# Kernel tuning notes

Hardware: AMD Instinct MI355X
Metric: run time of the kernel (lower is better)

The kernel has to match this reference:

```python
import jax, jax.numpy as jnp
import numpy as np

B, T, C, H, HD, START = 2, 2048, 2048, 16, 128, 1024


def setup_inputs() -> dict:
    key = jax.random.key(0)
    ks = jax.random.split(key, 8)
    x = jax.random.normal(ks[0], (B, T, C), dtype=jnp.float32)
    k_cache = jax.random.normal(ks[1], (B, H, START, HD), dtype=jnp.float32)
    v_cache = jax.random.normal(ks[2], (B, H, START, HD), dtype=jnp.float32)
    wq = jax.random.normal(ks[3], (C, C), dtype=jnp.float32) * 0.02
    wk = jax.random.normal(ks[4], (C, C), dtype=jnp.float32) * 0.02
    wv = jax.random.normal(ks[5], (C, C), dtype=jnp.float32) * 0.02
    wo = jax.random.normal(ks[6], (C, C), dtype=jnp.float32) * 0.02
    return {"x": x, "k_cache": k_cache, "v_cache": v_cache,
            "wq": wq, "wk": wk, "wv": wv, "wo": wo, "start_pos": START}


def reference(x, k_cache, v_cache, wq, wk, wv, wo, start_pos):
    b, t, c = x.shape
    h = k_cache.shape[1]
    hd = c // h
    scale = hd ** -0.5
    # projections (torch Linear: y = x @ W^T), split heads -> [B,H,T,hd]
    def proj(w):
        return jnp.einsum('btc,dc->btd', x, w).reshape(b, t, h, hd).transpose(0, 2, 1, 3)
    q = proj(wq)
    k_new = proj(wk)
    v_new = proj(wv)
    # cache update: full K,V over [0, start_pos+T)
    k = jnp.concatenate([k_cache, k_new], axis=2)  # [B,H,S,hd]
    v = jnp.concatenate([v_cache, v_new], axis=2)
    s = k.shape[2]
    attn = jnp.einsum('bhtd,bhsd->bhts', q, k) * scale  # [B,H,T,S]
    # causal mask: query i (absolute pos start_pos+i) may attend to j <= start_pos+i
    mask = jnp.arange(s)[None, :] > (jnp.arange(t)[:, None] + start_pos)
    attn = jnp.where(mask, -jnp.inf, attn)
    attn = jax.nn.softmax(attn, axis=-1)
    out = jnp.einsum('bhts,bhsd->bhtd', attn, v)
    out = out.transpose(0, 2, 1, 3).reshape(b, t, c)
    return jnp.einsum('btc,dc->btd', out, wo)
```

## Files before the change

### kernel.cpp

```cpp
#include <hip/hip_runtime.h>
#include <stdint.h>

typedef unsigned short u16;
typedef __attribute__((ext_vector_type(8))) short short8;
typedef __attribute__((ext_vector_type(4))) float f32x4;
typedef __attribute__((ext_vector_type(4))) u16 us4;
typedef __attribute__((ext_vector_type(8))) u16 us8;

#define DEVI static __device__ __forceinline__

constexpr int BB = 2, TQ = 2048, CD = 2048, NH = 16, HD = 128;
constexpr int STARTP = 1024, SK = 3072;
constexpr int MM = BB * TQ;
constexpr float SM_SCALE = 0.08838834764831845f;

DEVI u16 f2bf(float f) {
  union { float f; unsigned u; } v; v.f = f;
  return (u16)((v.u + 0x7fffu + ((v.u >> 16) & 1u)) >> 16);
}

typedef __attribute__((address_space(1))) const unsigned int gas_u32;
typedef __attribute__((address_space(3))) unsigned int las_u32;

DEVI void gload16(const void* g, void* l) {
  __builtin_amdgcn_global_load_lds((gas_u32*)(uintptr_t)g,
                                   (las_u32*)(unsigned)(uintptr_t)l, 16, 0, 0);
}


__global__ __launch_bounds__(256) void cvt_k(const float* __restrict__ in,
                                             u16* __restrict__ out, int n4) {
  int i = blockIdx.x * 256 + threadIdx.x, st = gridDim.x * 256;
  for (; i < n4; i += st) {
    float4 v = *(const float4*)(in + (size_t)i * 4);
    us4 o = { f2bf(v.x), f2bf(v.y), f2bf(v.z), f2bf(v.w) };
    *(us4*)(out + (size_t)i * 4) = o;
  }
}

__global__ __launch_bounds__(256) void kcache_k(const float* __restrict__ kc,
                                                u16* __restrict__ Kb) {
  constexpr int n4 = BB * NH * STARTP * HD / 4;
  int i = blockIdx.x * 256 + threadIdx.x, st = gridDim.x * 256;
  for (; i < n4; i += st) {
    int e = i * 4;
    int bh = e / (STARTP * HD);
    int rem = e - bh * (STARTP * HD);
    float4 v = *(const float4*)(kc + e);
    us4 o = { f2bf(v.x), f2bf(v.y), f2bf(v.z), f2bf(v.w) };
    *(us4*)(Kb + (size_t)bh * SK * HD + rem) = o;
  }
}

__global__ __launch_bounds__(256) void vcache_t_k(const float* __restrict__ vc,
                                                  u16* __restrict__ Vt) {
  __shared__ float tl[64][128];
  const int bh = blockIdx.y;
  const int s0 = blockIdx.x * 64;
  const int tid = threadIdx.x;
  const float* src = vc + ((size_t)bh * STARTP + s0) * HD;
  for (int it = 0; it < 32; ++it) {
    int flat = it * 256 + tid;
    tl[flat >> 7][flat & 127] = src[flat];
  }
  __syncthreads();
  int d = tid >> 1, half = tid & 1;
  u16* dst = Vt + ((size_t)bh * HD + d) * SK + s0 + half * 32;
#pragma unroll
  for (int c = 0; c < 4; ++c) {
    us8 v;
#pragma unroll
    for (int j = 0; j < 8; ++j) v[j] = f2bf(tl[half * 32 + c * 8 + j][d]);
    *(us8*)(dst + c * 8) = v;
  }
}

template <int MODE>
__global__ __launch_bounds__(256) void gemm_nt(
    const u16* __restrict__ A, const u16* __restrict__ W0,
    const u16* __restrict__ W1, const u16* __restrict__ W2,
    u16* __restrict__ Qb, u16* __restrict__ Kb, u16* __restrict__ Vtb,
    float* __restrict__ Co) {
  __shared__ __align__(16) u16 Alds[128 * 32];
  __shared__ __align__(16) u16 Blds[128 * 32];
  const int tid = threadIdx.x, lane = tid & 63, w = tid >> 6;
  const int wr = w >> 1, wc = w & 1;
  const int l15 = lane & 15, l4 = lane >> 4;
  const int m0 = blockIdx.x * 128;
  const int tn = blockIdx.y;
  const u16* Wp;
  int which = 0, nb;
  if (MODE == 0) {
    which = tn >> 4;
    nb = (tn & 15) * 128;
    Wp = which == 0 ? W0 : (which == 1 ? W1 : W2);
  } else {
    nb = tn * 128;
    Wp = W0;
  }

  const char* Ab = (const char*)(A + (size_t)m0 * CD);
  const char* Wb = (const char*)(Wp + (size_t)nb * CD);

  f32x4 acc[4][4] = {};

  for (int kt = 0; kt < CD * 2; kt += 64) {
    __syncthreads();
#pragma unroll
    for (int c = 0; c < 2; ++c) {
      int o = (w * 2 + c) * 1024 + lane * 16;
      int row = o >> 6, ib = o & 63;
      gload16(Ab + (size_t)row * 4096 + kt + ib, (char*)Alds + o);
      gload16(Wb + (size_t)row * 4096 + kt + ib, (char*)Blds + o);
    }
    asm volatile("s_waitcnt vmcnt(0)" ::: "memory");
    __syncthreads();
    short8 af[4], bfr[4];
#pragma unroll
    for (int i = 0; i < 4; ++i) {
      af[i]  = *(const short8*)((const char*)Alds + (wr * 64 + i * 16 + l15) * 64 + l4 * 16);
      bfr[i] = *(const short8*)((const char*)Blds + (wc * 64 + i * 16 + l15) * 64 + l4 * 16);
    }
#pragma unroll
    for (int i = 0; i < 4; ++i)
#pragma unroll
      for (int j = 0; j < 4; ++j)
        acc[i][j] = __builtin_amdgcn_mfma_f32_16x16x32_bf16(af[i], bfr[j], acc[i][j], 0, 0, 0);
  }

  const int r0 = m0 + wr * 64;
  const int c0 = nb + wc * 64;
#pragma unroll
  for (int i = 0; i < 4; ++i) {
#pragma unroll
    for (int j = 0; j < 4; ++j) {
      int mrow = r0 + i * 16 + l4 * 4;
      int ncol = c0 + j * 16 + l15;
      if (MODE == 1) {
#pragma unroll
        for (int r = 0; r < 4; ++r)
          Co[(size_t)(mrow + r) * 2048 + ncol] = acc[i][j][r];
      } else {
        int b = mrow >> 11;
        int t = mrow & 2047;
        int h = ncol >> 7, d = ncol & 127;
        int bh = b * NH + h;
        if (which == 0) {
          u16* p = Qb + ((size_t)bh * TQ + t) * HD + d;
#pragma unroll
          for (int r = 0; r < 4; ++r) p[r * HD] = f2bf(acc[i][j][r]);
        } else if (which == 1) {
          u16* p = Kb + ((size_t)bh * SK + STARTP + t) * HD + d;
#pragma unroll
          for (int r = 0; r < 4; ++r) p[r * HD] = f2bf(acc[i][j][r]);
        } else {
          us4 v = { f2bf(acc[i][j][0]), f2bf(acc[i][j][1]),
                    f2bf(acc[i][j][2]), f2bf(acc[i][j][3]) };
          *(us4*)(Vtb + ((size_t)bh * HD + d) * SK + STARTP + t) = v;
        }
      }
    }
  }
}

__global__ __launch_bounds__(256, 2) void attn_k(const u16* __restrict__ Qb,
                                                 const u16* __restrict__ Kb,
                                                 const u16* __restrict__ Vtb,
                                                 u16* __restrict__ AO) {
  __shared__ __align__(16) u16 Klds[64 * 128];
  __shared__ __align__(16) u16 Vlds[128 * 64];
  __shared__ __align__(16) u16 Plds[4][32 * 64];
  const int tid = threadIdx.x, lane = tid & 63, w = tid >> 6;
  const int l15 = lane & 15, l4 = lane >> 4;
  const int qt0 = blockIdx.x * 128;
  const int bh = blockIdx.y;

  short8 qf[2][4];
  const u16* Qbase = Qb + ((size_t)bh * TQ + qt0 + w * 32) * HD;
#pragma unroll
  for (int mi = 0; mi < 2; ++mi)
#pragma unroll
    for (int ks = 0; ks < 4; ++ks)
      qf[mi][ks] = *(const short8*)(Qbase + (mi * 16 + l15) * HD + ks * 32 + l4 * 8);

  f32x4 acc[2][8] = {};
  float mrun[2][4], lrun[2][4];
#pragma unroll
  for (int mi = 0; mi < 2; ++mi)
#pragma unroll
    for (int r = 0; r < 4; ++r) { mrun[mi][r] = -__builtin_inff(); lrun[mi][r] = 0.f; }

  const int nfull = (STARTP + qt0) >> 6;
  const int ntiles = nfull + 2;
  const char* Kg = (const char*)(Kb + (size_t)bh * SK * HD);
  const char* Vg = (const char*)(Vtb + (size_t)bh * HD * SK);
  char* Pl = (char*)Plds[w];

  for (int tt = 0; tt < ntiles; ++tt) {
    const int s0 = tt << 6;
    __syncthreads();
#pragma unroll
    for (int c = 0; c < 4; ++c) {
      int o = (w * 4 + c) * 1024 + lane * 16;
      int a = o ^ (((o >> 8) & 7) << 4);
      gload16(Kg + (size_t)s0 * 256 + a, (char*)Klds + o);
    }
#pragma unroll
    for (int c = 0; c < 4; ++c) {
      int o = (w * 4 + c) * 1024 + lane * 16;
      int a = o ^ (((o >> 7) & 7) << 4);
      int row = a >> 7, ib = a & 127;
      gload16(Vg + ((size_t)row * SK + s0) * 2 + ib, (char*)Vlds + o);
    }
    asm volatile("s_waitcnt vmcnt(0)" ::: "memory");
    __syncthreads();

    f32x4 sa[2][4] = {};
#pragma unroll
    for (int ks = 0; ks < 4; ++ks) {
      short8 kf[4];
#pragma unroll
      for (int ni = 0; ni < 4; ++ni) {
        int row = l15 + ni * 16;
        int a = row * 256 + ks * 64 + l4 * 16;
        kf[ni] = *(const short8*)((const char*)Klds + (a ^ ((row & 7) << 4)));
      }
#pragma unroll
      for (int mi = 0; mi < 2; ++mi)
#pragma unroll
        for (int ni = 0; ni < 4; ++ni)
          sa[mi][ni] = __builtin_amdgcn_mfma_f32_16x16x32_bf16(qf[mi][ks], kf[ni], sa[mi][ni], 0, 0, 0);
    }

    const bool need_mask = (tt >= nfull);
#pragma unroll
    for (int mi = 0; mi < 2; ++mi)
#pragma unroll
      for (int ni = 0; ni < 4; ++ni)
#pragma unroll
        for (int r = 0; r < 4; ++r) {
          float v = sa[mi][ni][r] * SM_SCALE;
          if (need_mask) {
            int col = s0 + ni * 16 + l15;
            int lim = STARTP + qt0 + w * 32 + mi * 16 + l4 * 4 + r;
            if (col > lim) v = -__builtin_inff();
          }
          sa[mi][ni][r] = v;
        }

#pragma unroll
    for (int mi = 0; mi < 2; ++mi) {
#pragma unroll
      for (int r = 0; r < 4; ++r) {
        float tmax = fmaxf(fmaxf(sa[mi][0][r], sa[mi][1][r]),
                           fmaxf(sa[mi][2][r], sa[mi][3][r]));
        tmax = fmaxf(tmax, __shfl_xor(tmax, 1));
        tmax = fmaxf(tmax, __shfl_xor(tmax, 2));
        tmax = fmaxf(tmax, __shfl_xor(tmax, 4));
        tmax = fmaxf(tmax, __shfl_xor(tmax, 8));
        float mnew = fmaxf(mrun[mi][r], tmax);
        float sf = __expf(mrun[mi][r] - mnew);
        mrun[mi][r] = mnew;
        float rs = 0.f;
#pragma unroll
        for (int ni = 0; ni < 4; ++ni) {
          float p = __expf(sa[mi][ni][r] - mnew);
          sa[mi][ni][r] = p;
          rs += p;
        }
        rs += __shfl_xor(rs, 1);
        rs += __shfl_xor(rs, 2);
        rs += __shfl_xor(rs, 4);
        rs += __shfl_xor(rs, 8);
        lrun[mi][r] = lrun[mi][r] * sf + rs;
#pragma unroll
        for (int ni = 0; ni < 8; ++ni) acc[mi][ni][r] *= sf;
      }
    }

#pragma unroll
    for (int mi = 0; mi < 2; ++mi)
#pragma unroll
      for (int ni = 0; ni < 4; ++ni)
#pragma unroll
        for (int r = 0; r < 4; ++r) {
          int row = mi * 16 + l4 * 4 + r;
          int col = ni * 16 + l15;
          int a = row * 128 + col * 2;
          *(u16*)(Pl + (a ^ ((row & 7) << 4))) = f2bf(sa[mi][ni][r]);
        }

#pragma unroll
    for (int ks = 0; ks < 2; ++ks) {
      short8 pf[2], vf[8];
#pragma unroll
      for (int mi = 0; mi < 2; ++mi) {
        int row = l15 + mi * 16;
        int a = row * 128 + ks * 64 + l4 * 16;
        pf[mi] = *(const short8*)(Pl + (a ^ ((row & 7) << 4)));
      }
#pragma unroll
      for (int ni = 0; ni < 8; ++ni) {
        int row = l15 + ni * 16;
        int a = row * 128 + ks * 64 + l4 * 16;
        vf[ni] = *(const short8*)((const char*)Vlds + (a ^ ((row & 7) << 4)));
      }
#pragma unroll
      for (int mi = 0; mi < 2; ++mi)
#pragma unroll
        for (int ni = 0; ni < 8; ++ni)
          acc[mi][ni] = __builtin_amdgcn_mfma_f32_16x16x32_bf16(pf[mi], vf[ni], acc[mi][ni], 0, 0, 0);
    }
  }

  const int b = bh >> 4, h = bh & 15;
#pragma unroll
  for (int mi = 0; mi < 2; ++mi) {
#pragma unroll
    for (int r = 0; r < 4; ++r) {
      float inv = 1.f / lrun[mi][r];
      int t = qt0 + w * 32 + mi * 16 + l4 * 4 + r;
      u16* dst = AO + ((size_t)(b * TQ + t)) * CD + h * HD + l15;
#pragma unroll
      for (int ni = 0; ni < 8; ++ni)
        dst[ni * 16] = f2bf(acc[mi][ni][r] * inv);
    }
  }
}


extern "C" void kernel_launch(void* const* d_in, const int* in_sizes, int n_in,
                              void* d_out, int out_size, void* d_ws, size_t ws_size,
                              hipStream_t stream) {
  const float* x  = (const float*)d_in[0];
  const float* kc = (const float*)d_in[1];
  const float* vc = (const float*)d_in[2];
  const float* wq = (const float*)d_in[3];
  const float* wk = (const float*)d_in[4];
  const float* wv = (const float*)d_in[5];
  const float* wo = (const float*)d_in[6];
  float* out = (float*)d_out;
  char* ws = (char*)d_ws;

  u16* xbf = (u16*)(ws);
  u16* AO  = (u16*)(ws);
  u16* wqb = (u16*)(ws + 16777216);
  u16* wkb = (u16*)(ws + 25165824);
  u16* wvb = (u16*)(ws + 33554432);
  u16* wob = (u16*)(ws + 41943040);
  u16* Qb  = (u16*)(ws + 50331648);
  u16* Kb  = (u16*)(ws + 67108864);
  u16* Vtb = (u16*)(ws + 92274688);

  cvt_k<<<2048, 256, 0, stream>>>(x, xbf, MM * CD / 4);
  cvt_k<<<1024, 256, 0, stream>>>(wq, wqb, CD * CD / 4);
  cvt_k<<<1024, 256, 0, stream>>>(wk, wkb, CD * CD / 4);
  cvt_k<<<1024, 256, 0, stream>>>(wv, wvb, CD * CD / 4);
  cvt_k<<<1024, 256, 0, stream>>>(wo, wob, CD * CD / 4);
  kcache_k<<<2048, 256, 0, stream>>>(kc, Kb);
  vcache_t_k<<<dim3(16, 32), 256, 0, stream>>>(vc, Vtb);

  gemm_nt<0><<<dim3(32, 48), 256, 0, stream>>>(xbf, wqb, wkb, wvb, Qb, Kb, Vtb, nullptr);
  attn_k<<<dim3(16, 32), 256, 0, stream>>>(Qb, Kb, Vtb, AO);
  gemm_nt<1><<<dim3(32, 16), 256, 0, stream>>>(AO, wob, nullptr, nullptr,
                                               nullptr, nullptr, nullptr, out);
}
```

Measured before the change: 602.0 us.

## Rework attention with paired causal tiles, double-buffered K/V, and lazy rescaling

The attention kernel now handles two 64-row query tiles per block, pairing tile qp with tile 31-qp so every block does the same amount of causal work. K/V tiles are double-buffered in LDS so the next tile's loads are issued while the current tile is computed. Softmax works in base 2 with exp2 and the scale folded in, and it only rescales the running max and accumulators when the new max exceeds the old by a threshold. The cost is smaller per-wave tiles (16 rows per wave), which lowers MFMA reuse of the loaded K/V, plus double the LDS and some extra control flow.

```diff
diff --git a/kernel.cpp b/kernel.cpp
--- a/kernel.cpp
+++ b/kernel.cpp
@@ -13,6 +13,7 @@
 constexpr int STARTP = 1024, SK = 3072;
 constexpr int MM = BB * TQ;
 constexpr float SM_SCALE = 0.08838834764831845f;
+constexpr float QSL2 = SM_SCALE * 1.4426950408889634f;
 
 DEVI u16 f2bf(float f) {
   union { float f; unsigned u; } v; v.f = f;
@@ -167,55 +168,90 @@
                                                  const u16* __restrict__ Kb,
                                                  const u16* __restrict__ Vtb,
                                                  u16* __restrict__ AO) {
-  __shared__ __align__(16) u16 Klds[64 * 128];
-  __shared__ __align__(16) u16 Vlds[128 * 64];
-  __shared__ __align__(16) u16 Plds[4][32 * 64];
+  __shared__ __align__(16) u16 Klds[2][64 * 128];
+  __shared__ __align__(16) u16 Vlds[2][128 * 64];
+  __shared__ __align__(16) u16 Plds[4][16 * 64];
   const int tid = threadIdx.x, lane = tid & 63, w = tid >> 6;
   const int l15 = lane & 15, l4 = lane >> 4;
-  const int qt0 = blockIdx.x * 128;
-  const int bh = blockIdx.y;
-
-  short8 qf[2][4];
-  const u16* Qbase = Qb + ((size_t)bh * TQ + qt0 + w * 32) * HD;
-#pragma unroll
-  for (int mi = 0; mi < 2; ++mi)
-#pragma unroll
-    for (int ks = 0; ks < 4; ++ks)
-      qf[mi][ks] = *(const short8*)(Qbase + (mi * 16 + l15) * HD + ks * 32 + l4 * 8);
-
-  f32x4 acc[2][8] = {};
-  float mrun[2][4], lrun[2][4];
-#pragma unroll
-  for (int mi = 0; mi < 2; ++mi)
-#pragma unroll
-    for (int r = 0; r < 4; ++r) { mrun[mi][r] = -__builtin_inff(); lrun[mi][r] = 0.f; }
-
-  const int nfull = (STARTP + qt0) >> 6;
-  const int ntiles = nfull + 2;
+  const int bh = blockIdx.x;
+  const int qp = blockIdx.y;
+  const int qt[2] = { qp, 31 - qp };
+  const int na = 17 + qp;
+  const int ntot = 65;
+
   const char* Kg = (const char*)(Kb + (size_t)bh * SK * HD);
   const char* Vg = (const char*)(Vtb + (size_t)bh * HD * SK);
   char* Pl = (char*)Plds[w];
 
-  for (int tt = 0; tt < ntiles; ++tt) {
-    const int s0 = tt << 6;
-    __syncthreads();
+  short8 qf[4];
+  f32x4 acc[8] = {};
+  float mrun[4], lrun[4];
+#pragma unroll
+  for (int r = 0; r < 4; ++r) { mrun[r] = -__builtin_inff(); lrun[r] = 0.f; }
+
+  auto LOADQ = [&](int seg) {
+    const u16* Qbase = Qb + ((size_t)bh * TQ + qt[seg] * 64 + w * 16 + l15) * HD;
+#pragma unroll
+    for (int ks = 0; ks < 4; ++ks)
+      qf[ks] = *(const short8*)(Qbase + ks * 32 + l4 * 8);
+  };
+
+  auto STAGE = [&](int buf, int s0) {
 #pragma unroll
     for (int c = 0; c < 4; ++c) {
       int o = (w * 4 + c) * 1024 + lane * 16;
-      int a = o ^ (((o >> 8) & 7) << 4);
-      gload16(Kg + (size_t)s0 * 256 + a, (char*)Klds + o);
-    }
-#pragma unroll
-    for (int c = 0; c < 4; ++c) {
-      int o = (w * 4 + c) * 1024 + lane * 16;
-      int a = o ^ (((o >> 7) & 7) << 4);
-      int row = a >> 7, ib = a & 127;
-      gload16(Vg + ((size_t)row * SK + s0) * 2 + ib, (char*)Vlds + o);
-    }
+      {
+        int a = o ^ (((o >> 8) & 7) << 4);
+        gload16(Kg + (size_t)s0 * 256 + a, (char*)Klds[buf] + o);
+      }
+      {
+        int a = o ^ (((o >> 7) & 7) << 4);
+        int row = a >> 7, ib = a & 127;
+        gload16(Vg + ((size_t)row * SK + s0) * 2 + ib, (char*)Vlds[buf] + o);
+      }
+    }
+  };
+
+  auto EPI = [&](int seg) {
+    const int b = bh >> 4, h = bh & 15;
+#pragma unroll
+    for (int r = 0; r < 4; ++r) {
+      float inv = 1.f / lrun[r];
+      int t = qt[seg] * 64 + w * 16 + l4 * 4 + r;
+      u16* dst = AO + ((size_t)(b * TQ + t)) * CD + h * HD + l15;
+#pragma unroll
+      for (int ni = 0; ni < 8; ++ni)
+        dst[ni * 16] = f2bf(acc[ni][r] * inv);
+    }
+  };
+
+  LOADQ(0);
+  STAGE(0, 0);
+  int cur = 0;
+
+  for (int t = 0; t < ntot; ++t) {
     asm volatile("s_waitcnt vmcnt(0)" ::: "memory");
     __syncthreads();
 
-    f32x4 sa[2][4] = {};
+    if (t + 1 < ntot) {
+      int nl = (t + 1 < na) ? (t + 1) : (t + 1 - na);
+      STAGE(cur ^ 1, nl << 6);
+    }
+
+    if (t == na) {
+      EPI(0);
+#pragma unroll
+      for (int ni = 0; ni < 8; ++ni) acc[ni] = f32x4{0.f, 0.f, 0.f, 0.f};
+#pragma unroll
+      for (int r = 0; r < 4; ++r) { mrun[r] = -__builtin_inff(); lrun[r] = 0.f; }
+      LOADQ(1);
+    }
+
+    const int loc = (t < na) ? t : t - na;
+    const int nseg = (t < na) ? na : ntot - na;
+    const bool diag = (loc == nseg - 1);
+
+    f32x4 sa[4] = {};
 #pragma unroll
     for (int ks = 0; ks < 4; ++ks) {
       short8 kf[4];
@@ -223,109 +259,97 @@
       for (int ni = 0; ni < 4; ++ni) {
         int row = l15 + ni * 16;
         int a = row * 256 + ks * 64 + l4 * 16;
-        kf[ni] = *(const short8*)((const char*)Klds + (a ^ ((row & 7) << 4)));
-      }
-#pragma unroll
-      for (int mi = 0; mi < 2; ++mi)
-#pragma unroll
-        for (int ni = 0; ni < 4; ++ni)
-          sa[mi][ni] = __builtin_amdgcn_mfma_f32_16x16x32_bf16(qf[mi][ks], kf[ni], sa[mi][ni], 0, 0, 0);
-    }
-
-    const bool need_mask = (tt >= nfull);
-#pragma unroll
-    for (int mi = 0; mi < 2; ++mi)
+        kf[ni] = *(const short8*)((const char*)Klds[cur] + (a ^ ((row & 7) << 4)));
+      }
 #pragma unroll
       for (int ni = 0; ni < 4; ++ni)
-#pragma unroll
-        for (int r = 0; r < 4; ++r) {
-          float v = sa[mi][ni][r] * SM_SCALE;
-          if (need_mask) {
-            int col = s0 + ni * 16 + l15;
-            int lim = STARTP + qt0 + w * 32 + mi * 16 + l4 * 4 + r;
-            if (col > lim) v = -__builtin_inff();
-          }
-          sa[mi][ni][r] = v;
+        sa[ni] = __builtin_amdgcn_mfma_f32_16x16x32_bf16(qf[ks], kf[ni], sa[ni], 0, 0, 0);
+    }
+
+#pragma unroll
+    for (int ni = 0; ni < 4; ++ni)
+#pragma unroll
+      for (int r = 0; r < 4; ++r) {
+        float v = sa[ni][r] * QSL2;
+        if (diag) {
+          int c = ni * 16 + l15;
+          int rr = w * 16 + l4 * 4 + r;
+          if (c > rr) v = -__builtin_inff();
         }
-
-#pragma unroll
-    for (int mi = 0; mi < 2; ++mi) {
+        sa[ni][r] = v;
+      }
+
+    float tmax[4];
+    bool need = false;
+#pragma unroll
+    for (int r = 0; r < 4; ++r) {
+      float m_ = fmaxf(fmaxf(sa[0][r], sa[1][r]), fmaxf(sa[2][r], sa[3][r]));
+      m_ = fmaxf(m_, __shfl_xor(m_, 1));
+      m_ = fmaxf(m_, __shfl_xor(m_, 2));
+      m_ = fmaxf(m_, __shfl_xor(m_, 4));
+      m_ = fmaxf(m_, __shfl_xor(m_, 8));
+      tmax[r] = m_;
+      need = need || (m_ > mrun[r] + 11.f);
+    }
+    if (__any(need)) {
 #pragma unroll
       for (int r = 0; r < 4; ++r) {
-        float tmax = fmaxf(fmaxf(sa[mi][0][r], sa[mi][1][r]),
-                           fmaxf(sa[mi][2][r], sa[mi][3][r]));
-        tmax = fmaxf(tmax, __shfl_xor(tmax, 1));
-        tmax = fmaxf(tmax, __shfl_xor(tmax, 2));
-        tmax = fmaxf(tmax, __shfl_xor(tmax, 4));
-        tmax = fmaxf(tmax, __shfl_xor(tmax, 8));
-        float mnew = fmaxf(mrun[mi][r], tmax);
-        float sf = __expf(mrun[mi][r] - mnew);
-        mrun[mi][r] = mnew;
-        float rs = 0.f;
-#pragma unroll
-        for (int ni = 0; ni < 4; ++ni) {
-          float p = __expf(sa[mi][ni][r] - mnew);
-          sa[mi][ni][r] = p;
-          rs += p;
-        }
-        rs += __shfl_xor(rs, 1);
-        rs += __shfl_xor(rs, 2);
-        rs += __shfl_xor(rs, 4);
-        rs += __shfl_xor(rs, 8);
-        lrun[mi][r] = lrun[mi][r] * sf + rs;
-#pragma unroll
-        for (int ni = 0; ni < 8; ++ni) acc[mi][ni][r] *= sf;
-      }
-    }
-
-#pragma unroll
-    for (int mi = 0; mi < 2; ++mi)
-#pragma unroll
-      for (int ni = 0; ni < 4; ++ni)
-#pragma unroll
-        for (int r = 0; r < 4; ++r) {
-          int row = mi * 16 + l4 * 4 + r;
-          int col = ni * 16 + l15;
-          int a = row * 128 + col * 2;
-          *(u16*)(Pl + (a ^ ((row & 7) << 4))) = f2bf(sa[mi][ni][r]);
-        }
+        float mn = fmaxf(mrun[r], tmax[r]);
+        float sf = __builtin_amdgcn_exp2f(mrun[r] - mn);
+        mrun[r] = mn;
+        lrun[r] *= sf;
+#pragma unroll
+        for (int ni = 0; ni < 8; ++ni) acc[ni][r] *= sf;
+      }
+    }
+#pragma unroll
+    for (int r = 0; r < 4; ++r) {
+      float rs = 0.f;
+#pragma unroll
+      for (int ni = 0; ni < 4; ++ni) {
+        float p = __builtin_amdgcn_exp2f(sa[ni][r] - mrun[r]);
+        sa[ni][r] = p;
+        rs += p;
+      }
+      rs += __shfl_xor(rs, 1);
+      rs += __shfl_xor(rs, 2);
+      rs += __shfl_xor(rs, 4);
+      rs += __shfl_xor(rs, 8);
+      lrun[r] += rs;
+    }
+
+#pragma unroll
+    for (int ni = 0; ni < 4; ++ni)
+#pragma unroll
+      for (int r = 0; r < 4; ++r) {
+        int row = l4 * 4 + r;
+        int col = ni * 16 + l15;
+        int a = row * 128 + col * 2;
+        *(u16*)(Pl + (a ^ ((row & 7) << 4))) = f2bf(sa[ni][r]);
+      }
 
 #pragma unroll
     for (int ks = 0; ks < 2; ++ks) {
-      short8 pf[2], vf[8];
-#pragma unroll
-      for (int mi = 0; mi < 2; ++mi) {
-        int row = l15 + mi * 16;
-        int a = row * 128 + ks * 64 + l4 * 16;
-        pf[mi] = *(const short8*)(Pl + (a ^ ((row & 7) << 4)));
+      short8 pf, vf[8];
+      {
+        int a = l15 * 128 + ks * 64 + l4 * 16;
+        pf = *(const short8*)(Pl + (a ^ ((l15 & 7) << 4)));
       }
 #pragma unroll
       for (int ni = 0; ni < 8; ++ni) {
         int row = l15 + ni * 16;
         int a = row * 128 + ks * 64 + l4 * 16;
-        vf[ni] = *(const short8*)((const char*)Vlds + (a ^ ((row & 7) << 4)));
-      }
-#pragma unroll
-      for (int mi = 0; mi < 2; ++mi)
-#pragma unroll
-        for (int ni = 0; ni < 8; ++ni)
-          acc[mi][ni] = __builtin_amdgcn_mfma_f32_16x16x32_bf16(pf[mi], vf[ni], acc[mi][ni], 0, 0, 0);
-    }
-  }
-
-  const int b = bh >> 4, h = bh & 15;
-#pragma unroll
-  for (int mi = 0; mi < 2; ++mi) {
-#pragma unroll
-    for (int r = 0; r < 4; ++r) {
-      float inv = 1.f / lrun[mi][r];
-      int t = qt0 + w * 32 + mi * 16 + l4 * 4 + r;
-      u16* dst = AO + ((size_t)(b * TQ + t)) * CD + h * HD + l15;
+        vf[ni] = *(const short8*)((const char*)Vlds[cur] + (a ^ ((row & 7) << 4)));
+      }
 #pragma unroll
       for (int ni = 0; ni < 8; ++ni)
-        dst[ni * 16] = f2bf(acc[mi][ni][r] * inv);
-    }
-  }
+        acc[ni] = __builtin_amdgcn_mfma_f32_16x16x32_bf16(pf, vf[ni], acc[ni], 0, 0, 0);
+    }
+
+    cur ^= 1;
+  }
+
+  EPI(1);
 }
 
 
@@ -361,7 +385,7 @@
   vcache_t_k<<<dim3(16, 32), 256, 0, stream>>>(vc, Vtb);
 
   gemm_nt<0><<<dim3(32, 48), 256, 0, stream>>>(xbf, wqb, wkb, wvb, Qb, Kb, Vtb, nullptr);
-  attn_k<<<dim3(16, 32), 256, 0, stream>>>(Qb, Kb, Vtb, AO);
+  attn_k<<<dim3(32, 16), 256, 0, stream>>>(Qb, Kb, Vtb, AO);
   gemm_nt<1><<<dim3(32, 16), 256, 0, stream>>>(AO, wob, nullptr, nullptr,
                                                nullptr, nullptr, nullptr, out);
 }
```

After: 502.3 us. 16.6% less time.
